# Kernel optimization log

Hardware: AMD Instinct MI355X
Metric: run time of the kernel (lower is better)

## Reference

```python
import jax, jax.numpy as jnp
import numpy as np


def setup_inputs() -> dict:
    key = jax.random.key(0)
    k1, k2, k3, k4 = jax.random.split(key, 4)
    b, c, h, w = 4, 256, 64, 64
    Fq_l = jax.random.normal(k1, (b, c, h, w), dtype=jnp.float32)
    Fp_l = jax.random.normal(k2, (b, c, h, w), dtype=jnp.float32)
    # 1x1 conv: weight [out=c//2, in=c], bias [c//2]
    W = jax.random.normal(k3, (c // 2, c), dtype=jnp.float32) * (1.0 / np.sqrt(c))
    bias = jax.random.normal(k4, (c // 2,), dtype=jnp.float32) * 0.01
    return {"Fq_l": Fq_l, "Fp_l": Fp_l, "W": W, "bias": bias}


def reference(Fq_l, Fp_l, W, bias):
    b, c, h, w = Fq_l.shape
    hw = h * w
    # 1x1 conv == per-pixel linear projection
    q = jnp.einsum('oc,bchw->bohw', W, Fq_l) + bias[None, :, None, None]
    p = jnp.einsum('oc,bchw->bohw', W, Fp_l) + bias[None, :, None, None]
    qf = q.reshape(b, -1, hw)  # [b, c/2, hw]
    pf = p.reshape(b, -1, hw)
    qf = qf / jnp.linalg.norm(qf, axis=1, keepdims=True)
    pf = pf / jnp.linalg.norm(pf, axis=1, keepdims=True)
    # cosine similarity, [b, hw, hw]
    sim = jnp.einsum('bcn,bcm->bnm', qf, pf)
    idx = jnp.argmax(sim, axis=-1)  # [b, hw]
    Fp_flat = Fp_l.reshape(b, c, hw)
    aligned = jnp.take_along_axis(Fp_flat, idx[:, None, :], axis=2)  # [b, c, hw]
    return aligned.reshape(b, c, h, w)
```

## Files before the change

### kernel.cpp

```cpp
#include <hip/hip_runtime.h>

#define HW 4096
#define LCAP 1536

typedef short bf16x8 __attribute__((ext_vector_type(8)));
typedef float f32x16 __attribute__((ext_vector_type(16)));

__device__ __forceinline__ ushort f2bf_rne(float f) {
    unsigned u = __float_as_uint(f);
    return (ushort)((u + 0x7FFFu + ((u >> 16) & 1u)) >> 16);
}

__global__ __launch_bounds__(256) void transpose_w_kernel(
    const float* __restrict__ Wm, float* __restrict__ Wt)
{
    const int o = blockIdx.x;
    const int c = threadIdx.x;
    Wt[c * 128 + o] = Wm[o * 256 + c];
}

__global__ __launch_bounds__(256) void proj_kernel(
    const float* __restrict__ Fq, const float* __restrict__ Fp,
    const float* __restrict__ Wt, const float* __restrict__ bias,
    float* __restrict__ Qt, float* __restrict__ Pt,
    ushort* __restrict__ Qpk, ushort* __restrict__ Ppk,
    float* __restrict__ qnorm)
{
    __shared__ float Ws[64][128];
    __shared__ float Xs[64][64];
    __shared__ float psum[16][68];

    const int tid = threadIdx.x;
    const int z  = blockIdx.z;
    const float* __restrict__ X = z ? Fp : Fq;
    const int b  = blockIdx.y;
    const int n0 = blockIdx.x * 64;
    const int og = tid >> 4;
    const int ng = tid & 15;

    float acc[4][8];
    #pragma unroll
    for (int i = 0; i < 4; ++i)
        #pragma unroll
        for (int j = 0; j < 8; ++j) acc[i][j] = 0.f;

    for (int cc = 0; cc < 4; ++cc) {
        __syncthreads();
        {
            const float4* src = (const float4*)(Wt + (size_t)cc * 64 * 128);
            float4* dst = (float4*)Ws;
            #pragma unroll
            for (int it = 0; it < 8; ++it) dst[it * 256 + tid] = src[it * 256 + tid];
        }
        #pragma unroll
        for (int it = 0; it < 4; ++it) {
            int f = it * 256 + tid;
            int r = f >> 4, n4 = f & 15;
            *(float4*)&Xs[r][n4 * 4] =
                *(const float4*)&X[(size_t)(b * 256 + cc * 64 + r) * HW + n0 + n4 * 4];
        }
        __syncthreads();

        for (int r = 0; r < 64; ++r) {
            float4 w0 = *(const float4*)&Ws[r][og * 8];
            float4 w1 = *(const float4*)&Ws[r][og * 8 + 4];
            float4 xv = *(const float4*)&Xs[r][ng * 4];
            float wa[8] = {w0.x, w0.y, w0.z, w0.w, w1.x, w1.y, w1.z, w1.w};
            float xa[4] = {xv.x, xv.y, xv.z, xv.w};
            #pragma unroll
            for (int i = 0; i < 4; ++i)
                #pragma unroll
                for (int j = 0; j < 8; ++j)
                    acc[i][j] += wa[j] * xa[i];
        }
    }

    {
        float4 b0 = *(const float4*)&bias[og * 8];
        float4 b1 = *(const float4*)&bias[og * 8 + 4];
        float ba[8] = {b0.x, b0.y, b0.z, b0.w, b1.x, b1.y, b1.z, b1.w};
        #pragma unroll
        for (int i = 0; i < 4; ++i)
            #pragma unroll
            for (int j = 0; j < 8; ++j) acc[i][j] += ba[j];
    }

    #pragma unroll
    for (int i = 0; i < 4; ++i) {
        float s = 0.f;
        #pragma unroll
        for (int j = 0; j < 8; ++j) s += acc[i][j] * acc[i][j];
        psum[og][ng * 4 + i] = s;
    }
    __syncthreads();
    float tot[4];
    #pragma unroll
    for (int i = 0; i < 4; ++i) {
        float s = 0.f;
        #pragma unroll
        for (int g = 0; g < 16; ++g) s += psum[g][ng * 4 + i];
        tot[i] = s;
    }

    if (z) {
        #pragma unroll
        for (int i = 0; i < 4; ++i) {
            float s = 1.0f / sqrtf(tot[i]);
            #pragma unroll
            for (int j = 0; j < 8; ++j) acc[i][j] *= s;
        }
    } else if (og == 0) {
        #pragma unroll
        for (int i = 0; i < 4; ++i)
            qnorm[b * HW + n0 + ng * 4 + i] = sqrtf(tot[i]);
    }

    {
        float* __restrict__ T = z ? Pt : Qt;
        #pragma unroll
        for (int i = 0; i < 4; ++i) {
            size_t tb = ((size_t)b * HW + n0 + ng * 4 + i) * 128 + og * 8;
            *(float4*)&T[tb]     = make_float4(acc[i][0], acc[i][1], acc[i][2], acc[i][3]);
            *(float4*)&T[tb + 4] = make_float4(acc[i][4], acc[i][5], acc[i][6], acc[i][7]);
        }
    }
    {
        ushort* __restrict__ PK = z ? Ppk : Qpk;
        const int ks = og >> 1;
        #pragma unroll
        for (int i = 0; i < 4; ++i) {
            const int na  = n0 + ng * 4 + i;
            const int t32 = na >> 5;
            const int lt  = (na & 31) + 32 * (og & 1);
            ushort u[8];
            #pragma unroll
            for (int k = 0; k < 8; ++k) u[k] = f2bf_rne(acc[i][k]);
            size_t pk = ((((size_t)b * 128 + t32) * 8 + ks) * 64 + lt) * 8;
            uint4 w;
            w.x = (unsigned)u[0] | ((unsigned)u[1] << 16);
            w.y = (unsigned)u[2] | ((unsigned)u[3] << 16);
            w.z = (unsigned)u[4] | ((unsigned)u[5] << 16);
            w.w = (unsigned)u[6] | ((unsigned)u[7] << 16);
            *(uint4*)&PK[pk] = w;
        }
    }
}

__global__ __launch_bounds__(256, 4) void sim_sketch_kernel(
    const ushort* __restrict__ Qpk, const ushort* __restrict__ Ppk,
    const float* __restrict__ qnorm, unsigned char* __restrict__ SK,
    unsigned char* __restrict__ BM)
{
    __shared__ ushort Bs[16384];

    const int tid  = threadIdx.x;
    const int lane = tid & 63;
    const int w    = tid >> 6;
    const int nb   = blockIdx.x;
    const int b    = blockIdx.y;
    const int ms   = blockIdx.z;
    const int hi   = lane >> 5;

    {
        const uint4* src = (const uint4*)(Ppk + ((size_t)(b * 128 + ms * 4)) * 4096);
        uint4* dst = (uint4*)Bs;
        #pragma unroll
        for (int it = 0; it < 8; ++it) dst[it * 256 + tid] = src[it * 256 + tid];
    }

    const ushort* __restrict__ qbase =
        Qpk + ((size_t)(b * 128 + nb * 4)) * 4096 + (size_t)lane * 8;
    bf16x8 qf[8];
    #pragma unroll
    for (int ks = 0; ks < 8; ++ks)
        qf[ks] = *(const bf16x8*)(qbase + (w * 8 + ks) * 512);

    float rq[16];
    #pragma unroll
    for (int r = 0; r < 16; ++r) {
        int nl_ = (r & 3) + 8 * (r >> 2) + 4 * hi;
        rq[r] = 256.0f / qnorm[b * HW + nb * 128 + w * 32 + nl_];
    }

    const size_t g16f = (size_t)b * 256 + (size_t)(nb * 4 + w) * 2 + hi;
    const int mb0 = ms * 128 + (lane & 31);

    float xmax[16];
    #pragma unroll
    for (int r = 0; r < 16; ++r) xmax[r] = -1e30f;

    __syncthreads();

    #pragma unroll 2
    for (int mtl = 0; mtl < 4; ++mtl) {
        f32x16 acc;
        #pragma unroll
        for (int r = 0; r < 16; ++r) acc[r] = 0.f;
        #pragma unroll
        for (int ks = 0; ks < 8; ++ks) {
            bf16x8 bb = *(const bf16x8*)&Bs[((mtl * 8 + ks) * 64 + lane) * 8];
            acc = __builtin_amdgcn_mfma_f32_32x32x16_bf16(qf[ks], bb, acc, 0, 0, 0);
        }

        unsigned dw[4] = {0u, 0u, 0u, 0u};
        #pragma unroll
        for (int r = 0; r < 16; ++r) {
            float x = acc[r] * rq[r];
            xmax[r] = fmaxf(xmax[r], x);
#if __has_builtin(__builtin_amdgcn_cvt_pk_u8_f32)
            dw[r >> 2] = (unsigned)__builtin_amdgcn_cvt_pk_u8_f32(
                x, (unsigned)(r & 3), (int)dw[r >> 2]);
#else
            int vi = (int)rintf(x);
            vi = vi < 0 ? 0 : (vi > 255 ? 255 : vi);
            dw[r >> 2] |= (unsigned)vi << (8 * (r & 3));
#endif
        }
        const int m = mb0 + mtl * 32;
        uint4 pk;
        pk.x = dw[0]; pk.y = dw[1]; pk.z = dw[2]; pk.w = dw[3];
        *(uint4*)(SK + ((g16f * 4096 + (size_t)m) << 4)) = pk;
    }

    #pragma unroll
    for (int r = 0; r < 16; ++r) {
        float v = xmax[r];
        #pragma unroll
        for (int d = 1; d < 32; d <<= 1)
            v = fmaxf(v, __shfl_xor(v, d, 64));
        xmax[r] = v;
    }
    if ((lane & 31) == 0) {
        unsigned dw[4] = {0u, 0u, 0u, 0u};
        #pragma unroll
        for (int r = 0; r < 16; ++r) {
#if __has_builtin(__builtin_amdgcn_cvt_pk_u8_f32)
            dw[r >> 2] = (unsigned)__builtin_amdgcn_cvt_pk_u8_f32(
                xmax[r], (unsigned)(r & 3), (int)dw[r >> 2]);
#else
            int vi = (int)rintf(xmax[r]);
            vi = vi < 0 ? 0 : (vi > 255 ? 255 : vi);
            dw[r >> 2] |= (unsigned)vi << (8 * (r & 3));
#endif
        }
        uint4 pk;
        pk.x = dw[0]; pk.y = dw[1]; pk.z = dw[2]; pk.w = dw[3];
        *(uint4*)(BM + ((g16f * 32 + (size_t)ms) << 4)) = pk;
    }
}

__device__ __noinline__ void dot_one_slow(
    const float* Qsrow, const float* __restrict__ Pt,
    int b, int m, int n, unsigned long long* __restrict__ best)
{
    const float4* __restrict__ pr = (const float4*)&Pt[((size_t)b * HW + m) * 128];
    float acc = 0.f;
    #pragma unroll
    for (int k = 0; k < 32; ++k) {
        float4 pv = pr[k];
        float4 qv = *(const float4*)&Qsrow[k * 4];
        acc += qv.x * pv.x + qv.y * pv.y + qv.z * pv.z + qv.w * pv.w;
    }
    unsigned u = __float_as_uint(acc);
    unsigned kk = (u & 0x80000000u) ? ~u : (u | 0x80000000u);
    unsigned long long key = ((unsigned long long)kk << 32) | (unsigned)(4095 - m);
    atomicMax(&best[(size_t)b * HW + n], key);
}

__global__ __launch_bounds__(256) void scan_rescore_kernel(
    const unsigned char* __restrict__ SK, const unsigned char* __restrict__ BM,
    const float* __restrict__ Qt, const float* __restrict__ Pt,
    unsigned long long* __restrict__ best)
{
    __shared__ float Qs[16][132];
    __shared__ int nlist[16];
    __shared__ int t8s[16];
    __shared__ ushort hl[LCAP];
    __shared__ unsigned lcnt;

    const int fg  = blockIdx.x;
    const int tid = threadIdx.x;
    const int b = fg >> 8, g = fg & 255, t = g >> 1, gs = g & 1;

    if (tid == 0) lcnt = 0u;
    if (tid < 16) {
        int n = t * 32 + (tid & 3) + 8 * (tid >> 2) + 4 * gs;
        nlist[tid] = n;
        best[(size_t)b * HW + n] = 0ull;
        const unsigned char* __restrict__ bmrow = BM + ((size_t)fg << 9);
        int mc = 0;
        #pragma unroll
        for (int ms = 0; ms < 32; ++ms)
            mc = max(mc, (int)bmrow[ms * 16 + tid]);
        int tt = mc - 6;
        t8s[tid] = tt < 0 ? 0 : tt;
    }
    __syncthreads();

    #pragma unroll
    for (int it = 0; it < 2; ++it) {
        int idx = it * 256 + tid;
        int row = idx >> 5, c4 = (idx & 31) * 4;
        *(float4*)&Qs[row][c4] =
            *(const float4*)&Qt[((size_t)b * HW + nlist[row]) * 128 + c4];
    }

    int myt[16];
    #pragma unroll
    for (int j = 0; j < 16; ++j) myt[j] = t8s[j];
    unsigned tw[4];
    #pragma unroll
    for (int d = 0; d < 4; ++d)
        tw[d] = (unsigned)myt[d * 4]
              | ((unsigned)myt[d * 4 + 1] << 8)
              | ((unsigned)myt[d * 4 + 2] << 16)
              | ((unsigned)myt[d * 4 + 3] << 24);
    __syncthreads();

    const uint4* __restrict__ skrow = (const uint4*)(SK + ((size_t)fg << 16));
    const unsigned H = 0x80808080u;

    #pragma unroll 4
    for (int it = 0; it < 16; ++it) {
        const int m = it * 256 + tid;
        uint4 v = skrow[it * 256 + tid];
        unsigned wv[4] = {v.x, v.y, v.z, v.w};
        unsigned ge[4];
        #pragma unroll
        for (int d = 0; d < 4; ++d) {
            unsigned x = wv[d], y = tw[d];
            unsigned L = (x | H) - (y & ~H);
            ge[d] = ((x & ~y) | (~(x ^ y) & L)) & H;
        }
        if (ge[0] | ge[1] | ge[2] | ge[3]) {
            #pragma unroll
            for (int d = 0; d < 4; ++d) {
                if (ge[d]) {
                    #pragma unroll
                    for (int k = 0; k < 4; ++k) {
                        if (ge[d] & (0x80u << (8 * k))) {
                            int j = d * 4 + k;
                            unsigned pos = atomicAdd(&lcnt, 1u);
                            if (pos < LCAP) {
                                hl[pos] = (ushort)((j << 12) | m);
                            } else {
                                dot_one_slow(&Qs[j][0], Pt, b, m, nlist[j], best);
                            }
                        }
                    }
                }
            }
        }
    }

    __syncthreads();
    unsigned cnt = lcnt < LCAP ? lcnt : LCAP;
    for (unsigned p = tid; p < cnt; p += 256) {
        int e = hl[p];
        int j = e >> 12, m = e & 4095;
        const float4* __restrict__ pr = (const float4*)&Pt[((size_t)b * HW + m) * 128];
        float acc = 0.f;
        #pragma unroll
        for (int k = 0; k < 32; ++k) {
            float4 pv = pr[k];
            float4 qv = *(const float4*)&Qs[j][k * 4];
            acc += qv.x * pv.x + qv.y * pv.y + qv.z * pv.z + qv.w * pv.w;
        }
        unsigned u = __float_as_uint(acc);
        unsigned kk = (u & 0x80000000u) ? ~u : (u | 0x80000000u);
        unsigned long long key = ((unsigned long long)kk << 32) | (unsigned)(4095 - m);
        atomicMax(&best[(size_t)b * HW + nlist[j]], key);
    }
}

__global__ __launch_bounds__(256) void gather_kernel(
    const float* __restrict__ Fp, const unsigned long long* __restrict__ best,
    float* __restrict__ out)
{
    __shared__ float row[4096];
    const int blk = blockIdx.x;
    const int c = blk & 255;
    const int b = blk >> 8;
    const int tid = threadIdx.x;

    const float* __restrict__ src = Fp + ((size_t)b * 256 + c) * HW;
    #pragma unroll
    for (int it = 0; it < 4; ++it) {
        int f = it * 256 + tid;
        *(float4*)&row[f * 4] = *(const float4*)&src[f * 4];
    }
    __syncthreads();

    float* __restrict__ dst = out + ((size_t)b * 256 + c) * HW;
    #pragma unroll
    for (int it = 0; it < 16; ++it) {
        int n = it * 256 + tid;
        int m = 4095 - (int)(best[(size_t)b * HW + n] & 0xFFFull);
        dst[n] = row[m];
    }
}

extern "C" void kernel_launch(void* const* d_in, const int* in_sizes, int n_in,
                              void* d_out, int out_size, void* d_ws, size_t ws_size,
                              hipStream_t stream) {
    const float* Fq   = (const float*)d_in[0];
    const float* Fp   = (const float*)d_in[1];
    const float* Wm   = (const float*)d_in[2];
    const float* bias = (const float*)d_in[3];
    float* out = (float*)d_out;

    char* base = (char*)d_ws;
    float*  Qt    = (float*)(base);
    float*  Pt    = (float*)(base + (8u << 20));
    ushort* Qpk   = (ushort*)(base + (16u << 20));
    ushort* Ppk   = (ushort*)(base + (20u << 20));
    unsigned char* SK = (unsigned char*)(base + (24u << 20));
    char* x = base + (88u << 20);
    unsigned char* BM = (unsigned char*)x;  x += 524288;
    float*  qnorm = (float*)x;              x += 65536;
    unsigned long long* best = (unsigned long long*)x; x += 131072;
    float*  Wtg   = (float*)x;

    transpose_w_kernel<<<128, 256, 0, stream>>>(Wm, Wtg);
    proj_kernel<<<dim3(64, 4, 2), 256, 0, stream>>>(Fq, Fp, Wtg, bias,
                                                    Qt, Pt, Qpk, Ppk, qnorm);
    sim_sketch_kernel<<<dim3(32, 4, 32), 256, 0, stream>>>(Qpk, Ppk, qnorm,
                                                           SK, BM);
    scan_rescore_kernel<<<1024, 256, 0, stream>>>(SK, BM, Qt, Pt, best);
    gather_kernel<<<1024, 256, 0, stream>>>(Fp, best, out);
}
```

Baseline: 166.2 us.

## Fold query norm scaling into bf16 packing and prefetch projection chunks into registers

The 256/||q|| scale is now applied to the packed bf16 query before the similarity MFMA, which removes the qnorm buffer, its per-thread loads, and the 16 multiplies per tile in the sketch kernel. In the projection kernel, the loads of the next weight and input chunk are software-pipelined into registers so global loads overlap the FMA loop. The prescaled bf16 values have a different rounding point, which could slightly perturb the u8 sketch. Holding the prefetched chunk needs extra registers.

```diff
diff --git a/kernel.cpp b/kernel.cpp
--- a/kernel.cpp
+++ b/kernel.cpp
@@ -23,8 +23,7 @@
     const float* __restrict__ Fq, const float* __restrict__ Fp,
     const float* __restrict__ Wt, const float* __restrict__ bias,
     float* __restrict__ Qt, float* __restrict__ Pt,
-    ushort* __restrict__ Qpk, ushort* __restrict__ Ppk,
-    float* __restrict__ qnorm)
+    ushort* __restrict__ Qpk, ushort* __restrict__ Ppk)
 {
     __shared__ float Ws[64][128];
     __shared__ float Xs[64][64];
@@ -44,28 +43,51 @@
         #pragma unroll
         for (int j = 0; j < 8; ++j) acc[i][j] = 0.f;
 
+    float4 w0, w1, w2, w3, w4, w5, w6, w7;
+    float4 x0, x1, x2, x3;
+    const int xr0 = tid >> 4,            xn0 = (tid & 15) * 4;
+    const int xr1 = (256 + tid) >> 4,    xn1 = xn0;
+    const int xr2 = (512 + tid) >> 4,    xn2 = xn0;
+    const int xr3 = (768 + tid) >> 4,    xn3 = xn0;
+
+#define LOAD_CHUNK(cc_)                                                        \
+    {                                                                          \
+        const float4* s_ = (const float4*)(Wt + (size_t)(cc_) * 64 * 128);     \
+        w0 = s_[0 * 256 + tid]; w1 = s_[1 * 256 + tid];                        \
+        w2 = s_[2 * 256 + tid]; w3 = s_[3 * 256 + tid];                        \
+        w4 = s_[4 * 256 + tid]; w5 = s_[5 * 256 + tid];                        \
+        w6 = s_[6 * 256 + tid]; w7 = s_[7 * 256 + tid];                        \
+        const size_t cb_ = (size_t)(b * 256 + (cc_) * 64);                     \
+        x0 = *(const float4*)&X[(cb_ + xr0) * HW + n0 + xn0];                  \
+        x1 = *(const float4*)&X[(cb_ + xr1) * HW + n0 + xn1];                  \
+        x2 = *(const float4*)&X[(cb_ + xr2) * HW + n0 + xn2];                  \
+        x3 = *(const float4*)&X[(cb_ + xr3) * HW + n0 + xn3];                  \
+    }
+
+    LOAD_CHUNK(0);
+
     for (int cc = 0; cc < 4; ++cc) {
         __syncthreads();
         {
-            const float4* src = (const float4*)(Wt + (size_t)cc * 64 * 128);
             float4* dst = (float4*)Ws;
-            #pragma unroll
-            for (int it = 0; it < 8; ++it) dst[it * 256 + tid] = src[it * 256 + tid];
-        }
-        #pragma unroll
-        for (int it = 0; it < 4; ++it) {
-            int f = it * 256 + tid;
-            int r = f >> 4, n4 = f & 15;
-            *(float4*)&Xs[r][n4 * 4] =
-                *(const float4*)&X[(size_t)(b * 256 + cc * 64 + r) * HW + n0 + n4 * 4];
-        }
+            dst[0 * 256 + tid] = w0; dst[1 * 256 + tid] = w1;
+            dst[2 * 256 + tid] = w2; dst[3 * 256 + tid] = w3;
+            dst[4 * 256 + tid] = w4; dst[5 * 256 + tid] = w5;
+            dst[6 * 256 + tid] = w6; dst[7 * 256 + tid] = w7;
+        }
+        *(float4*)&Xs[xr0][xn0] = x0;
+        *(float4*)&Xs[xr1][xn1] = x1;
+        *(float4*)&Xs[xr2][xn2] = x2;
+        *(float4*)&Xs[xr3][xn3] = x3;
         __syncthreads();
 
+        if (cc < 3) LOAD_CHUNK(cc + 1);
+
         for (int r = 0; r < 64; ++r) {
-            float4 w0 = *(const float4*)&Ws[r][og * 8];
-            float4 w1 = *(const float4*)&Ws[r][og * 8 + 4];
+            float4 a0 = *(const float4*)&Ws[r][og * 8];
+            float4 a1 = *(const float4*)&Ws[r][og * 8 + 4];
             float4 xv = *(const float4*)&Xs[r][ng * 4];
-            float wa[8] = {w0.x, w0.y, w0.z, w0.w, w1.x, w1.y, w1.z, w1.w};
+            float wa[8] = {a0.x, a0.y, a0.z, a0.w, a1.x, a1.y, a1.z, a1.w};
             float xa[4] = {xv.x, xv.y, xv.z, xv.w};
             #pragma unroll
             for (int i = 0; i < 4; ++i)
@@ -74,6 +96,7 @@
                     acc[i][j] += wa[j] * xa[i];
         }
     }
+#undef LOAD_CHUNK
 
     {
         float4 b0 = *(const float4*)&bias[og * 8];
@@ -102,17 +125,18 @@
         tot[i] = s;
     }
 
+    float pscale[4];
     if (z) {
         #pragma unroll
         for (int i = 0; i < 4; ++i) {
             float s = 1.0f / sqrtf(tot[i]);
             #pragma unroll
             for (int j = 0; j < 8; ++j) acc[i][j] *= s;
-        }
-    } else if (og == 0) {
-        #pragma unroll
-        for (int i = 0; i < 4; ++i)
-            qnorm[b * HW + n0 + ng * 4 + i] = sqrtf(tot[i]);
+            pscale[i] = 1.0f;
+        }
+    } else {
+        #pragma unroll
+        for (int i = 0; i < 4; ++i) pscale[i] = 256.0f / sqrtf(tot[i]);
     }
 
     {
@@ -134,7 +158,7 @@
             const int lt  = (na & 31) + 32 * (og & 1);
             ushort u[8];
             #pragma unroll
-            for (int k = 0; k < 8; ++k) u[k] = f2bf_rne(acc[i][k]);
+            for (int k = 0; k < 8; ++k) u[k] = f2bf_rne(acc[i][k] * pscale[i]);
             size_t pk = ((((size_t)b * 128 + t32) * 8 + ks) * 64 + lt) * 8;
             uint4 w;
             w.x = (unsigned)u[0] | ((unsigned)u[1] << 16);
@@ -148,8 +172,7 @@
 
 __global__ __launch_bounds__(256, 4) void sim_sketch_kernel(
     const ushort* __restrict__ Qpk, const ushort* __restrict__ Ppk,
-    const float* __restrict__ qnorm, unsigned char* __restrict__ SK,
-    unsigned char* __restrict__ BM)
+    unsigned char* __restrict__ SK, unsigned char* __restrict__ BM)
 {
     __shared__ ushort Bs[16384];
 
@@ -175,13 +198,6 @@
     for (int ks = 0; ks < 8; ++ks)
         qf[ks] = *(const bf16x8*)(qbase + (w * 8 + ks) * 512);
 
-    float rq[16];
-    #pragma unroll
-    for (int r = 0; r < 16; ++r) {
-        int nl_ = (r & 3) + 8 * (r >> 2) + 4 * hi;
-        rq[r] = 256.0f / qnorm[b * HW + nb * 128 + w * 32 + nl_];
-    }
-
     const size_t g16f = (size_t)b * 256 + (size_t)(nb * 4 + w) * 2 + hi;
     const int mb0 = ms * 128 + (lane & 31);
 
@@ -205,7 +221,7 @@
         unsigned dw[4] = {0u, 0u, 0u, 0u};
         #pragma unroll
         for (int r = 0; r < 16; ++r) {
-            float x = acc[r] * rq[r];
+            float x = acc[r];
             xmax[r] = fmaxf(xmax[r], x);
 #if __has_builtin(__builtin_amdgcn_cvt_pk_u8_f32)
             dw[r >> 2] = (unsigned)__builtin_amdgcn_cvt_pk_u8_f32(
@@ -417,15 +433,13 @@
     unsigned char* SK = (unsigned char*)(base + (24u << 20));
     char* x = base + (88u << 20);
     unsigned char* BM = (unsigned char*)x;  x += 524288;
-    float*  qnorm = (float*)x;              x += 65536;
     unsigned long long* best = (unsigned long long*)x; x += 131072;
     float*  Wtg   = (float*)x;
 
     transpose_w_kernel<<<128, 256, 0, stream>>>(Wm, Wtg);
     proj_kernel<<<dim3(64, 4, 2), 256, 0, stream>>>(Fq, Fp, Wtg, bias,
-                                                    Qt, Pt, Qpk, Ppk, qnorm);
-    sim_sketch_kernel<<<dim3(32, 4, 32), 256, 0, stream>>>(Qpk, Ppk, qnorm,
-                                                           SK, BM);
+                                                    Qt, Pt, Qpk, Ppk);
+    sim_sketch_kernel<<<dim3(32, 4, 32), 256, 0, stream>>>(Qpk, Ppk, SK, BM);
     scan_rescore_kernel<<<1024, 256, 0, stream>>>(SK, BM, Qt, Pt, best);
     gather_kernel<<<1024, 256, 0, stream>>>(Fp, best, out);
 }
```

After: 170.5 us (median of 2 runs). 2.5% more time.
